# Kernel tuning notes

Hardware: AMD Instinct MI355X
Metric: run time of the kernel (lower is better)

## Reference

```python
import jax, jax.numpy as jnp
import numpy as np

N = 50000      # nodes
E = 800000     # edges (avg degree 16)
DIN = 256      # input_dim
DH = 128       # hidden_dim
ALPHA_LOGIT = 0.6190392084062235  # logit(0.65)


def setup_inputs() -> dict:
    key = jax.random.key(0)
    ks = jax.random.split(key, 12)
    f = lambda k, s: jax.random.normal(k, s, dtype=jnp.float32)
    return {
        "x": f(ks[0], (N, DIN)),
        "edge_index": jax.random.randint(ks[1], (2, E), 0, N, dtype=jnp.int32),
        "reranker_scores": f(ks[2], (N,)),
        # input_proj
        "Wp": f(ks[3], (DIN, DH)) * 0.02, "bp": jnp.zeros((DH,), jnp.float32),
        # SAGEConv 0: lin_l (aggregated neighbors, with bias), lin_r (root, no bias)
        "Wl0": f(ks[4], (DIN, DH)) * 0.02, "bl0": jnp.zeros((DH,), jnp.float32),
        "Wr0": f(ks[5], (DIN, DH)) * 0.02,
        # SAGEConv 1
        "Wl1": f(ks[6], (DH, DH)) * 0.02, "bl1": jnp.zeros((DH,), jnp.float32),
        "Wr1": f(ks[7], (DH, DH)) * 0.02,
        # score head MLP
        "W1": f(ks[8], (DH, DH // 2)) * 0.02, "b1": jnp.zeros((DH // 2,), jnp.float32),
        "W2": f(ks[9], (DH // 2, 1)) * 0.02, "b2": jnp.zeros((1,), jnp.float32),
        "alpha_logit": jnp.float32(ALPHA_LOGIT),
    }


def _sage_conv(h, src, dst, Wl, bl, Wr):
    # PyG SAGEConv (aggr='mean', root_weight=True):
    # out = lin_l(mean_{j in N(i)} h_j) + lin_r(h_i)
    msg = h[src]                                             # [E, d] gather
    agg = jax.ops.segment_sum(msg, dst, num_segments=N)      # [N, d]
    cnt = jax.ops.segment_sum(jnp.ones((src.shape[0],), h.dtype), dst, num_segments=N)
    agg = agg / jnp.maximum(cnt, 1.0)[:, None]               # mean; isolated nodes -> 0
    return agg @ Wl + bl + h @ Wr


def reference(x, edge_index, reranker_scores, Wp, bp, Wl0, bl0, Wr0,
              Wl1, bl1, Wr1, W1, b1, W2, b2, alpha_logit):
    src, dst = edge_index[0], edge_index[1]
    # norm_type='none' -> no input normalization; eval mode -> dropout is identity
    residual = x @ Wp + bp                                   # [N, DH]
    h = jax.nn.relu(_sage_conv(x, src, dst, Wl0, bl0, Wr0)) + residual
    h = jax.nn.relu(_sage_conv(h, src, dst, Wl1, bl1, Wr1)) + h
    gnn_scores = (jax.nn.relu(h @ W1 + b1) @ W2 + b2)[:, 0]  # [N]
    alpha = jax.nn.sigmoid(alpha_logit)
    return alpha * reranker_scores + (1.0 - alpha) * gnn_scores
```

## Files before the change

kernel.cpp:

```cpp
#include <hip/hip_runtime.h>
#include <hip/hip_bf16.h>


#define DIN 256
#define DH 128
#define NPB 256
#define LOG_NPB 8
#define NBMAX 256
#define EPB 2048
#define JL (EPB/256)
#define SLOTS 8192

typedef __attribute__((ext_vector_type(8))) short short8;
typedef __attribute__((ext_vector_type(4))) float float4v;
typedef __attribute__((ext_vector_type(2))) float float2v;

__device__ inline ushort f2b(float f){
  unsigned u = __float_as_uint(f);
  u = (u + 0x7fffu + ((u >> 16) & 1u)) >> 16;
  return (ushort)u;
}
__device__ inline float blo(unsigned v){ return __uint_as_float(v << 16); }
__device__ inline float bhi(unsigned v){ return __uint_as_float(v & 0xffff0000u); }
__device__ inline short8 pack8(float4 f0, float4 f1){
  short8 v;
  v[0]=(short)f2b(f0.x); v[1]=(short)f2b(f0.y); v[2]=(short)f2b(f0.z); v[3]=(short)f2b(f0.w);
  v[4]=(short)f2b(f1.x); v[5]=(short)f2b(f1.y); v[6]=(short)f2b(f1.z); v[7]=(short)f2b(f1.w);
  return v;
}
__device__ inline void glds16(const ushort* g, ushort* l){
  __builtin_amdgcn_global_load_lds((const __attribute__((address_space(1))) void*)g,
                                   (__attribute__((address_space(3))) void*)l, 16, 0, 0);
}
__device__ inline unsigned char enc8(float v){
  return (unsigned char)(__builtin_amdgcn_cvt_pk_fp8_f32(v, v, 0, false) & 0xFF);
}
__device__ inline float2v dec8(unsigned u){
  return __builtin_amdgcn_cvt_pk_f32_fp8((int)u, false);
}

__device__ inline void gather16x2(const ushort* __restrict__ a8,
    const int* __restrict__ adj, int pA, int eA, int pB, int eB, int lane,
    float& a0A, float& a1A, float& a0B, float& a1B)
{
  while (pA < eA || pB < eB){
    ushort uA[16], uB[16];
    bool dA = pA < eA, dB = pB < eB;
    if (dA){
      #pragma unroll
      for (int j=0;j<16;j++) uA[j] = a8[(size_t)adj[pA+j]*64 + lane];
    }
    if (dB){
      #pragma unroll
      for (int j=0;j<16;j++) uB[j] = a8[(size_t)adj[pB+j]*64 + lane];
    }
    if (dA){
      #pragma unroll
      for (int j=0;j<16;j++){ float2v f = dec8(uA[j]); a0A += f[0]; a1A += f[1]; }
      pA += 16;
    }
    if (dB){
      #pragma unroll
      for (int j=0;j<16;j++){ float2v f = dec8(uB[j]); a0B += f[0]; a1B += f[1]; }
      pB += 16;
    }
  }
}

__global__ __launch_bounds__(256) void fused_front(
    const float* __restrict__ x, int N, ushort* __restrict__ xb, int nstripe,
    const float* __restrict__ Wp, const float* __restrict__ Wl0, const float* __restrict__ Wr0,
    const float* __restrict__ Wl1, const float* __restrict__ Wr1, const float* __restrict__ W1,
    ushort* __restrict__ Wpf, ushort* __restrict__ Wl0f, ushort* __restrict__ Wr0f,
    ushort* __restrict__ Wl1f, ushort* __restrict__ Wr1f, ushort* __restrict__ W1f,
    const int* __restrict__ src, const int* __restrict__ dst, int E, int NB,
    int* __restrict__ bucketCnt, int* __restrict__ pairS, int* __restrict__ pairD,
    int nPart, int nConv)
{
  __shared__ int hist[NBMAX], lbase[NBMAX], gbase[NBMAX], lcur[NBMAX], sc[NBMAX];
  __shared__ int ls[EPB], ld[EPB];
  int bid = blockIdx.x;
  int t = threadIdx.x;

  if (bid < nPart){
    int base = bid * EPB;
    int cntE = E - base; if (cntE > EPB) cntE = EPB;
    for (int i=t;i<NB;i+=256) hist[i]=0;
    __syncthreads();
    int myS[JL], myD[JL];
    #pragma unroll
    for (int j=0;j<JL;j++){
      int e = base + j*256 + t;
      if (e < E){ myS[j]=src[e]; myD[j]=dst[e]; atomicAdd(&hist[myD[j]>>LOG_NPB],1); }
      else myD[j] = -1;
    }
    __syncthreads();
    if (t < NBMAX) sc[t] = (t < NB)? hist[t] : 0;
    __syncthreads();
    for (int st=1; st<NBMAX; st<<=1){
      int v = 0;
      if (t < NBMAX && t >= st) v = sc[t-st];
      __syncthreads();
      if (t < NBMAX) sc[t] += v;
      __syncthreads();
    }
    if (t < NB){
      int excl = (t>0)? sc[t-1] : 0;
      lbase[t] = excl; lcur[t] = excl;
      gbase[t] = atomicAdd(&bucketCnt[t], hist[t]);
    }
    __syncthreads();
    #pragma unroll
    for (int j=0;j<JL;j++){
      if (myD[j] >= 0){
        int b = myD[j] >> LOG_NPB;
        int p = atomicAdd(&lcur[b], 1);
        ls[p] = myS[j]; ld[p] = myD[j];
      }
    }
    __syncthreads();
    for (int i=t;i<cntE;i+=256){
      int d = ld[i];
      int b = d >> LOG_NPB;
      int p = gbase[b] + (i - lbase[b]);
      if (p < SLOTS){
        pairS[(size_t)b*SLOTS + p] = ls[i];
        pairD[(size_t)b*SLOTS + p] = d;
      }
    }
  } else if (bid < nPart + nConv){
    int gi = (bid - nPart)*256 + t;
    if (gi < nstripe*512){
      int L = gi & 63, ks = (gi>>6)&7, s = gi>>9;
      int row = s*16 + (L&15);
      int k = ks*32 + (L>>4)*8;
      short8 v;
      if (row < N){
        const float* p = x + (size_t)row*DIN + k;
        v = pack8(*(const float4*)p, *(const float4*)(p+4));
      } else {
        #pragma unroll
        for (int j=0;j<8;j++) v[j]=0;
      }
      *(short8*)(xb + (size_t)gi*8) = v;
    }
  } else {
    int gi = (bid - nPart - nConv)*256 + t;
    if (gi < 17408){
      const float* sw; ushort* dw; int cols, b0;
      if      (gi <  4096){ sw=Wp;  dw=Wpf;  cols=128; b0=0; }
      else if (gi <  8192){ sw=Wl0; dw=Wl0f; cols=128; b0=4096; }
      else if (gi < 12288){ sw=Wr0; dw=Wr0f; cols=128; b0=8192; }
      else if (gi < 14336){ sw=Wl1; dw=Wl1f; cols=128; b0=12288; }
      else if (gi < 16384){ sw=Wr1; dw=Wr1f; cols=128; b0=14336; }
      else                { sw=W1;  dw=W1f;  cols=64;  b0=16384; }
      int i = gi - b0;
      int ln = i & 63, g = i >> 6;
      int ntq = cols >> 4;
      int nt = g % ntq, ks = g / ntq;
      int col = nt*16 + (ln & 15);
      int k0 = ks*32 + (ln >> 4)*8;
      short8 v;
      #pragma unroll
      for (int j=0;j<8;j++) v[j] = (short)f2b(sw[(size_t)(k0+j)*cols + col]);
      *(short8*)(dw + (size_t)i*8) = v;
    }
  }
}

__global__ __launch_bounds__(256) void gemm0_csr(
    const ushort* __restrict__ xb, int N, int nstripe, int ngemm, int nbuck,
    const ushort* __restrict__ Wpf, const ushort* __restrict__ Wl0f, const ushort* __restrict__ Wr0f,
    const float* __restrict__ bp,
    ushort* __restrict__ xp, unsigned char* __restrict__ q8, ushort* __restrict__ xr0,
    const int* __restrict__ bucketCnt, const int* __restrict__ pairS, const int* __restrict__ pairD,
    int* __restrict__ off, int* __restrict__ deg, int* __restrict__ adj)
{
  __shared__ __align__(16) ushort smem[32768];
  int bid = blockIdx.x, t = threadIdx.x;

  if (bid >= nbuck){
    int g = bid - nbuck;
    int xcd = g & 7, jj = g >> 3;
    int mat = jj % 3;
    int b = xcd + 8*(jj/3);
    int nblk = ngemm / 3;
    const ushort* Wf = (mat==0)? Wpf : (mat==1)? Wl0f : Wr0f;
    int w = t>>6, lane = t&63, lq = lane&15, quad = lane>>4;
    #pragma unroll
    for (int j=0;j<16;j++){
      int gg = w + j*4;
      glds16(Wf + (size_t)gg*512 + lane*8, smem + gg*512);
    }
    __syncthreads();
    float bias[8];
    #pragma unroll
    for (int nt=0;nt<8;nt++) bias[nt] = (mat==0)? bp[nt*16 + lq] : 0.f;
    int nchunk = (nstripe + 3) >> 2;

#define LOADAV(AV, cc) do { \
    int stripe_ = (cc)*4 + w; \
    if (stripe_ < nstripe){ \
      _Pragma("unroll") \
      for (int ks=0;ks<8;ks++) \
        AV[ks] = *(const short8*)(xb + ((size_t)stripe_*8 + ks)*512 + lane*8); \
    } \
  } while(0)

#define COMPSTORE(AV, cc) do { \
    int stripe_ = (cc)*4 + w; \
    if (stripe_ < nstripe){ \
      int row0_ = stripe_*16; \
      float4v acc_[8]; \
      _Pragma("unroll") for (int nt=0;nt<8;nt++){ \
        _Pragma("unroll") for (int r=0;r<4;r++) acc_[nt][r]=0.f; } \
      _Pragma("unroll") for (int ks=0;ks<8;ks++){ \
        _Pragma("unroll") for (int nt=0;nt<8;nt++){ \
          short8 bf_ = *(const short8*)(smem + (size_t)((ks*8+nt)*64 + lane)*8); \
          acc_[nt] = __builtin_amdgcn_mfma_f32_16x16x32_bf16(AV[ks], bf_, acc_[nt], 0,0,0); \
        } \
      } \
      if (mat == 1){ \
        _Pragma("unroll") for (int nt=0;nt<8;nt++) \
        _Pragma("unroll") for (int r=0;r<4;r++){ \
          int row_ = row0_ + quad*4 + r; \
          if (row_ < N) q8[(size_t)row_*128 + nt*16 + lq] = enc8(acc_[nt][r]); \
        } \
      } else { \
        ushort* Y_ = (mat==0)? xp : xr0; \
        _Pragma("unroll") for (int nt=0;nt<8;nt++) \
        _Pragma("unroll") for (int r=0;r<4;r++){ \
          int row_ = row0_ + quad*4 + r; \
          if (row_ < N) Y_[(size_t)row_*128 + nt*16 + lq] = f2b(acc_[nt][r] + bias[nt]); \
        } \
      } \
    } \
  } while(0)

    short8 avA[8], avB[8];
    int c = b;
    if (c < nchunk){
      LOADAV(avA, c);
      while (true){
        int cn = c + nblk;
        if (cn < nchunk) LOADAV(avB, cn);
        COMPSTORE(avA, c);
        c = cn;
        if (c >= nchunk) break;
        cn = c + nblk;
        if (cn < nchunk) LOADAV(avA, cn);
        COMPSTORE(avB, c);
        c = cn;
        if (c >= nchunk) break;
      }
    }
#undef LOADAV
#undef COMPSTORE
  } else {
    int b = bid;
    int* cnt  = (int*)smem;
    int* offl = cnt + 256;
    int* s1   = offl + 257;
    int* win  = s1 + 256;
    int node0 = b * NPB;
    int base  = b * SLOTS;
    int ce = bucketCnt[b]; if (ce > SLOTS) ce = SLOTS;
    int ce4 = ce & ~3;
    cnt[t] = 0;
    __syncthreads();
    for (int i = t*4; i < ce4; i += 1024){
      int4 dd = *(const int4*)(pairD + base + i);
      atomicAdd(&cnt[dd.x - node0], 1);
      atomicAdd(&cnt[dd.y - node0], 1);
      atomicAdd(&cnt[dd.z - node0], 1);
      atomicAdd(&cnt[dd.w - node0], 1);
    }
    for (int i = ce4 + t; i < ce; i += 256)
      atomicAdd(&cnt[pairD[(size_t)base+i] - node0], 1);
    __syncthreads();
    int a = cnt[t];
    int pa = (a + 15) & ~15;
    s1[t] = pa;
    __syncthreads();
    for (int st=1; st<256; st<<=1){
      int v = (t>=st)? s1[t-st] : 0;
      __syncthreads();
      s1[t] += v;
      __syncthreads();
    }
    int excl = (t>0)? s1[t-1] : 0;
    offl[t] = excl;
    int ptotal = s1[255]; if (ptotal > SLOTS) ptotal = SLOTS;
    int node = node0 + t;
    if (node < N){ off[node] = base + excl; deg[node] = a; }
    __syncthreads();
    for (int i=t;i<ptotal;i+=256) win[i] = N;
    __syncthreads();
    for (int i = t*4; i < ce4; i += 1024){
      int4 dd = *(const int4*)(pairD + base + i);
      int4 ss = *(const int4*)(pairS + base + i);
      int p0 = atomicAdd(&offl[dd.x - node0], 1); if (p0 < SLOTS) win[p0] = ss.x;
      int p1 = atomicAdd(&offl[dd.y - node0], 1); if (p1 < SLOTS) win[p1] = ss.y;
      int p2 = atomicAdd(&offl[dd.z - node0], 1); if (p2 < SLOTS) win[p2] = ss.z;
      int p3 = atomicAdd(&offl[dd.w - node0], 1); if (p3 < SLOTS) win[p3] = ss.w;
    }
    for (int i = ce4 + t; i < ce; i += 256){
      int dd = pairD[(size_t)base+i];
      int p = atomicAdd(&offl[dd - node0], 1);
      if (p < SLOTS) win[p] = pairS[(size_t)base+i];
    }
    __syncthreads();
    for (int i=t;i<ptotal;i+=256) adj[(size_t)base+i] = win[i];
  }
}

__global__ __launch_bounds__(256) void combine0_f8(
    const unsigned char* __restrict__ agg8, const ushort* __restrict__ rootsrc,
    const ushort* __restrict__ ressrc, const float* __restrict__ bias,
    const int* __restrict__ off, const int* __restrict__ deg,
    const int* __restrict__ adj, ushort* __restrict__ out, int n)
{
  int t = threadIdx.x;
  int d = t & 63, w = t >> 6;
  int nA = blockIdx.x*8 + w*2, nB = nA + 1;
  if (nA >= n) return;
  const ushort* a8 = (const ushort*)agg8;
  bool vB = nB < n;
  unsigned rtA = ((const unsigned*)rootsrc)[(size_t)nA*64 + d];
  unsigned rsA = ((const unsigned*)ressrc)[(size_t)nA*64 + d];
  unsigned rtB = 0, rsB = 0;
  int pA = off[nA], cA = deg[nA], eA = pA + ((cA + 15) & ~15);
  int pB = 0, cB = 0, eB = 0;
  if (vB){
    rtB = ((const unsigned*)rootsrc)[(size_t)nB*64 + d];
    rsB = ((const unsigned*)ressrc)[(size_t)nB*64 + d];
    pB = off[nB]; cB = deg[nB]; eB = pB + ((cB + 15) & ~15);
  }
  float a0A=0.f, a1A=0.f, a0B=0.f, a1B=0.f;
  gather16x2(a8, adj, pA, eA, pB, eB, d, a0A, a1A, a0B, a1B);
  float b0 = bias[2*d], b1v = bias[2*d+1];
  float invA = 1.f / (float)((cA > 1)? cA : 1);
  float o0 = fmaxf(a0A*invA + b0  + blo(rtA), 0.f) + blo(rsA);
  float o1 = fmaxf(a1A*invA + b1v + bhi(rtA), 0.f) + bhi(rsA);
  ((unsigned*)out)[(size_t)nA*64 + d] = (unsigned)f2b(o0) | ((unsigned)f2b(o1) << 16);
  if (vB){
    float invB = 1.f / (float)((cB > 1)? cB : 1);
    float q0 = fmaxf(a0B*invB + b0  + blo(rtB), 0.f) + blo(rsB);
    float q1 = fmaxf(a1B*invB + b1v + bhi(rtB), 0.f) + bhi(rsB);
    ((unsigned*)out)[(size_t)nB*64 + d] = (unsigned)f2b(q0) | ((unsigned)f2b(q1) << 16);
  }
}

__global__ __launch_bounds__(256) void gemm1_wres(
    const ushort* __restrict__ h, int N,
    const ushort* __restrict__ Wl1f, const ushort* __restrict__ Wr1f,
    unsigned char* __restrict__ q8, ushort* __restrict__ hr1)
{
  __shared__ __align__(16) ushort Bs[32768];
  int t = threadIdx.x, w = t>>6, lane = t&63, lq = lane&15, quad = lane>>4;
  int tile = blockIdx.x;
  #pragma unroll
  for (int j=0;j<16;j++){
    int r = w + j*4;
    int m = r>>5, g = r&31;
    const ushort* Wm = m ? Wr1f : Wl1f;
    glds16(Wm + (size_t)g*512 + lane*8, Bs + r*512);
  }
  short8 av[2][4];
  int row0 = tile*128 + w*32;
  #pragma unroll
  for (int mt=0;mt<2;mt++){
    int row = row0 + mt*16 + lq; if (row >= N) row = N-1;
    #pragma unroll
    for (int ks=0;ks<4;ks++)
      av[mt][ks] = *(const short8*)(h + (size_t)row*128 + ks*32 + quad*8);
  }
  __syncthreads();
  #pragma unroll
  for (int m=0;m<2;m++){
    float4v acc[2][8];
    #pragma unroll
    for (int i=0;i<2;i++)
      #pragma unroll
      for (int j=0;j<8;j++)
        #pragma unroll
        for (int r=0;r<4;r++) acc[i][j][r] = 0.f;
    #pragma unroll
    for (int ks=0;ks<4;ks++){
      #pragma unroll
      for (int nt=0;nt<8;nt++){
        short8 bf = *(const short8*)(Bs + ((m*32 + ks*8 + nt)*64 + lane)*8);
        acc[0][nt] = __builtin_amdgcn_mfma_f32_16x16x32_bf16(av[0][ks], bf, acc[0][nt], 0,0,0);
        acc[1][nt] = __builtin_amdgcn_mfma_f32_16x16x32_bf16(av[1][ks], bf, acc[1][nt], 0,0,0);
      }
    }
    #pragma unroll
    for (int mt=0;mt<2;mt++){
      #pragma unroll
      for (int r=0;r<4;r++){
        int row = row0 + mt*16 + quad*4 + r;
        if (row < N){
          if (m == 0){
            #pragma unroll
            for (int nt=0;nt<8;nt++)
              q8[(size_t)row*128 + nt*16 + lq] = enc8(acc[mt][nt][r]);
          } else {
            #pragma unroll
            for (int nt=0;nt<8;nt++)
              hr1[(size_t)row*128 + nt*16 + lq] = f2b(acc[mt][nt][r]);
          }
        }
      }
    }
  }
}

__global__ __launch_bounds__(256) void combine1_head(
    const unsigned char* __restrict__ agg8, const ushort* __restrict__ hr1,
    const ushort* __restrict__ h, const float* __restrict__ bl1,
    const int* __restrict__ off, const int* __restrict__ deg, const int* __restrict__ adj,
    const ushort* __restrict__ W1f, const float* __restrict__ b1,
    const float* __restrict__ W2, const float* __restrict__ b2,
    const float* __restrict__ alogit, const float* __restrict__ rer,
    float* __restrict__ out, int n)
{
  __shared__ __align__(16) ushort W1s[8192];
  __shared__ __align__(16) ushort h2s[16*136];
  int t = threadIdx.x, w = t>>6, lane = t&63, lq = lane&15, quad = lane>>4;
  #pragma unroll
  for (int j=0;j<4;j++){
    int g = w + j*4;
    glds16(W1f + (size_t)g*512 + lane*8, W1s + g*512);
  }
  int node0 = blockIdx.x*16;
  unsigned* h2u = (unsigned*)h2s;
  const ushort* a8 = (const ushort*)agg8;
  float bb0 = bl1[2*lane], bb1 = bl1[2*lane+1];
  #pragma unroll
  for (int jp=0;jp<2;jp++){
    int nA = node0 + w*4 + jp*2, nB = nA + 1;
    bool vA = nA < n, vB = nB < n;
    unsigned rtA=0, rsA=0, rtB=0, rsB=0;
    int pA=0, eA=0, cA=0, pB=0, eB=0, cB=0;
    if (vA){
      rtA = ((const unsigned*)hr1)[(size_t)nA*64 + lane];
      rsA = ((const unsigned*)h  )[(size_t)nA*64 + lane];
      pA = off[nA]; cA = deg[nA]; eA = pA + ((cA + 15) & ~15);
    }
    if (vB){
      rtB = ((const unsigned*)hr1)[(size_t)nB*64 + lane];
      rsB = ((const unsigned*)h  )[(size_t)nB*64 + lane];
      pB = off[nB]; cB = deg[nB]; eB = pB + ((cB + 15) & ~15);
    }
    float a0A=0.f, a1A=0.f, a0B=0.f, a1B=0.f;
    gather16x2(a8, adj, pA, eA, pB, eB, lane, a0A, a1A, a0B, a1B);
    float o0A=0.f, o1A=0.f, o0B=0.f, o1B=0.f;
    if (vA){
      float inv = 1.f / (float)((cA > 1)? cA : 1);
      o0A = fmaxf(a0A*inv + bb0 + blo(rtA), 0.f) + blo(rsA);
      o1A = fmaxf(a1A*inv + bb1 + bhi(rtA), 0.f) + bhi(rsA);
    }
    if (vB){
      float inv = 1.f / (float)((cB > 1)? cB : 1);
      o0B = fmaxf(a0B*inv + bb0 + blo(rtB), 0.f) + blo(rsB);
      o1B = fmaxf(a1B*inv + bb1 + bhi(rtB), 0.f) + bhi(rsB);
    }
    h2u[(w*4 + jp*2    )*68 + lane] = (unsigned)f2b(o0A) | ((unsigned)f2b(o1A) << 16);
    h2u[(w*4 + jp*2 + 1)*68 + lane] = (unsigned)f2b(o0B) | ((unsigned)f2b(o1B) << 16);
  }
  __syncthreads();

  short8 av[4];
  #pragma unroll
  for (int ks=0;ks<4;ks++)
    av[ks] = *(const short8*)(h2s + lq*136 + ks*32 + quad*8);
  float4v acc[4];
  #pragma unroll
  for (int nt=0;nt<4;nt++)
    #pragma unroll
    for (int r=0;r<4;r++) acc[nt][r] = 0.f;
  #pragma unroll
  for (int ks=0;ks<4;ks++){
    #pragma unroll
    for (int nt=0;nt<4;nt++){
      short8 bf = *(const short8*)(W1s + ((ks*4 + nt)*64 + lane)*8);
      acc[nt] = __builtin_amdgcn_mfma_f32_16x16x32_bf16(av[ks], bf, acc[nt], 0,0,0);
    }
  }
  float al = alogit[0];
  float a  = 1.f / (1.f + __expf(-al));
  float pw[4] = {0.f,0.f,0.f,0.f};
  #pragma unroll
  for (int nt=0; nt<4; nt++){
    int c = nt*16 + lq;
    float w2 = W2[c];
    float bb = b1[c];
    #pragma unroll
    for (int r=0; r<4; r++)
      pw[r] += fmaxf(acc[nt][r] + bb, 0.f) * w2;
  }
  #pragma unroll
  for (int mask=1; mask<16; mask<<=1){
    #pragma unroll
    for (int r=0; r<4; r++)
      pw[r] += __shfl_xor(pw[r], mask);
  }
  if (lq == 0){
    #pragma unroll
    for (int r=0; r<4; r++){
      int rl = quad*4 + r;
      if ((rl >> 2) == w){
        int node = node0 + rl;
        if (node < n)
          out[node] = a * rer[node] + (1.f - a) * (pw[r] + b2[0]);
      }
    }
  }
}

extern "C" void kernel_launch(void* const* d_in, const int* in_sizes, int n_in,
                              void* d_out, int out_size, void* d_ws, size_t ws_size,
                              hipStream_t stream)
{
  (void)n_in; (void)out_size; (void)ws_size;
  const float* x    = (const float*)d_in[0];
  const int*   ei   = (const int*)d_in[1];
  const float* rer  = (const float*)d_in[2];
  const float* Wp   = (const float*)d_in[3];
  const float* bp   = (const float*)d_in[4];
  const float* Wl0  = (const float*)d_in[5];
  const float* bl0  = (const float*)d_in[6];
  const float* Wr0  = (const float*)d_in[7];
  const float* Wl1  = (const float*)d_in[8];
  const float* bl1  = (const float*)d_in[9];
  const float* Wr1  = (const float*)d_in[10];
  const float* W1   = (const float*)d_in[11];
  const float* b1   = (const float*)d_in[12];
  const float* W2   = (const float*)d_in[13];
  const float* b2   = (const float*)d_in[14];
  const float* alogit = (const float*)d_in[15];

  const int N = in_sizes[2];
  const int E = in_sizes[1] / 2;
  const int* src = ei;
  const int* dst = ei + E;
  const int NB = (N + NPB - 1) / NPB;
  const int nstripe = (N + 15) / 16;
  const int ntile = (N + 127) / 128;
  const int nPart = (E + EPB - 1) / EPB;
  const int nConv = (nstripe*512 + 255)/256;

  ushort* U = (ushort*)d_ws;
  ushort* xb  = U;
  ushort* xp  = xb + (size_t)nstripe*512*8;
  ushort* xr0 = xp  + (size_t)N*DH;
  ushort* h   = xr0 + (size_t)N*DH;
  unsigned char* q8 = (unsigned char*)(h + (size_t)N*DH);
  ushort* Wpf  = (ushort*)(q8 + (size_t)(N+1)*DH);
  ushort* Wl0f = Wpf  + (size_t)4096*8;
  ushort* Wr0f = Wl0f + (size_t)4096*8;
  ushort* Wl1f = Wr0f + (size_t)4096*8;
  ushort* Wr1f = Wl1f + (size_t)2048*8;
  ushort* W1f  = Wr1f + (size_t)2048*8;
  int* I = (int*)(W1f + (size_t)1024*8);
  int* bucketCnt = I;
  int* off   = bucketCnt + NBMAX;
  int* deg   = off + N;
  int* pairS = deg + N;
  int* pairD = pairS + (size_t)NB*SLOTS;
  int* adj   = pairD + (size_t)NB*SLOTS;

  hipMemsetAsync(bucketCnt, 0, NBMAX*sizeof(int), stream);
  hipMemsetAsync(q8 + (size_t)N*DH, 0, DH, stream);

  fused_front<<<nPart + nConv + 68, 256, 0, stream>>>(
      x, N, xb, nstripe, Wp, Wl0, Wr0, Wl1, Wr1, W1,
      Wpf, Wl0f, Wr0f, Wl1f, Wr1f, W1f,
      src, dst, E, NB, bucketCnt, pairS, pairD, nPart, nConv);

  gemm0_csr<<<NB + 768, 256, 0, stream>>>(
      xb, N, nstripe, 768, NB, Wpf, Wl0f, Wr0f, bp, xp, q8, xr0,
      bucketCnt, pairS, pairD, off, deg, adj);

  combine0_f8<<<(N+7)/8, 256, 0, stream>>>(q8, xr0, xp, bl0, off, deg, adj, h, N);

  gemm1_wres<<<ntile, 256, 0, stream>>>(h, N, Wl1f, Wr1f, q8, xr0);

  combine1_head<<<(N+15)/16, 256, 0, stream>>>(
      q8, xr0, h, bl1, off, deg, adj, W1f, b1, W2, b2, alogit, rer, (float*)d_out, N);
}
```

Baseline: 228.0 us.

## Split each wavefront into half-waves gathering 4-byte fp8 rows per lane

```diff
diff --git a/kernel.cpp b/kernel.cpp
--- a/kernel.cpp
+++ b/kernel.cpp
@@ -35,35 +35,47 @@
 __device__ inline unsigned char enc8(float v){
   return (unsigned char)(__builtin_amdgcn_cvt_pk_fp8_f32(v, v, 0, false) & 0xFF);
 }
-__device__ inline float2v dec8(unsigned u){
+__device__ inline float2v dec8lo(unsigned u){
   return __builtin_amdgcn_cvt_pk_f32_fp8((int)u, false);
 }
-
-__device__ inline void gather16x2(const ushort* __restrict__ a8,
-    const int* __restrict__ adj, int pA, int eA, int pB, int eB, int lane,
-    float& a0A, float& a1A, float& a0B, float& a1B)
+__device__ inline float2v dec8hi(unsigned u){
+  return __builtin_amdgcn_cvt_pk_f32_fp8((int)u, true);
+}
+
+__device__ inline void gather_sw(const unsigned* __restrict__ a8u,
+    const int* __restrict__ adj, int zrow, int ln,
+    int pP, int eP, int pQ, int eQ,
+    float* accP, float* accQ)
 {
-  while (pA < eA || pB < eB){
-    ushort uA[16], uB[16];
-    bool dA = pA < eA, dB = pB < eB;
-    if (dA){
-      #pragma unroll
-      for (int j=0;j<16;j++) uA[j] = a8[(size_t)adj[pA+j]*64 + lane];
-    }
-    if (dB){
-      #pragma unroll
-      for (int j=0;j<16;j++) uB[j] = a8[(size_t)adj[pB+j]*64 + lane];
-    }
-    if (dA){
-      #pragma unroll
-      for (int j=0;j<16;j++){ float2v f = dec8(uA[j]); a0A += f[0]; a1A += f[1]; }
-      pA += 16;
-    }
-    if (dB){
-      #pragma unroll
-      for (int j=0;j<16;j++){ float2v f = dec8(uB[j]); a0B += f[0]; a1B += f[1]; }
-      pB += 16;
-    }
+  int rem = eP - pP; int remQ = eQ - pQ; if (remQ > rem) rem = remQ;
+  #pragma unroll
+  for (int m=1; m<64; m<<=1){ int o = __shfl_xor(rem, m); if (o > rem) rem = o; }
+  int iters = rem >> 4;
+  for (int it=0; it<iters; ++it){
+    bool aP = pP < eP, aQ = pQ < eQ;
+    unsigned uP[16], uQ[16];
+    #pragma unroll
+    for (int j=0;j<16;j++){
+      int ix = zrow; if (aP) ix = adj[pP+j];
+      uP[j] = a8u[(size_t)ix*32 + ln];
+    }
+    #pragma unroll
+    for (int j=0;j<16;j++){
+      int ix = zrow; if (aQ) ix = adj[pQ+j];
+      uQ[j] = a8u[(size_t)ix*32 + ln];
+    }
+    #pragma unroll
+    for (int j=0;j<16;j++){
+      float2v f0 = dec8lo(uP[j]), f1 = dec8hi(uP[j]);
+      accP[0]+=f0[0]; accP[1]+=f0[1]; accP[2]+=f1[0]; accP[3]+=f1[1];
+    }
+    #pragma unroll
+    for (int j=0;j<16;j++){
+      float2v f0 = dec8lo(uQ[j]), f1 = dec8hi(uQ[j]);
+      accQ[0]+=f0[0]; accQ[1]+=f0[1]; accQ[2]+=f1[0]; accQ[3]+=f1[1];
+    }
+    if (aP) pP += 16;
+    if (aQ) pQ += 16;
   }
 }
 
@@ -320,34 +332,49 @@
     const int* __restrict__ off, const int* __restrict__ deg,
     const int* __restrict__ adj, ushort* __restrict__ out, int n)
 {
-  int t = threadIdx.x;
-  int d = t & 63, w = t >> 6;
-  int nA = blockIdx.x*8 + w*2, nB = nA + 1;
-  if (nA >= n) return;
-  const ushort* a8 = (const ushort*)agg8;
-  bool vB = nB < n;
-  unsigned rtA = ((const unsigned*)rootsrc)[(size_t)nA*64 + d];
-  unsigned rsA = ((const unsigned*)ressrc)[(size_t)nA*64 + d];
-  unsigned rtB = 0, rsB = 0;
-  int pA = off[nA], cA = deg[nA], eA = pA + ((cA + 15) & ~15);
-  int pB = 0, cB = 0, eB = 0;
-  if (vB){
-    rtB = ((const unsigned*)rootsrc)[(size_t)nB*64 + d];
-    rsB = ((const unsigned*)ressrc)[(size_t)nB*64 + d];
-    pB = off[nB]; cB = deg[nB]; eB = pB + ((cB + 15) & ~15);
-  }
-  float a0A=0.f, a1A=0.f, a0B=0.f, a1B=0.f;
-  gather16x2(a8, adj, pA, eA, pB, eB, d, a0A, a1A, a0B, a1B);
-  float b0 = bias[2*d], b1v = bias[2*d+1];
-  float invA = 1.f / (float)((cA > 1)? cA : 1);
-  float o0 = fmaxf(a0A*invA + b0  + blo(rtA), 0.f) + blo(rsA);
-  float o1 = fmaxf(a1A*invA + b1v + bhi(rtA), 0.f) + bhi(rsA);
-  ((unsigned*)out)[(size_t)nA*64 + d] = (unsigned)f2b(o0) | ((unsigned)f2b(o1) << 16);
-  if (vB){
-    float invB = 1.f / (float)((cB > 1)? cB : 1);
-    float q0 = fmaxf(a0B*invB + b0  + blo(rtB), 0.f) + blo(rsB);
-    float q1 = fmaxf(a1B*invB + b1v + bhi(rtB), 0.f) + bhi(rsB);
-    ((unsigned*)out)[(size_t)nB*64 + d] = (unsigned)f2b(q0) | ((unsigned)f2b(q1) << 16);
+  int t = threadIdx.x, w = t>>6, lane = t&63, ln = lane&31, sel = lane>>5;
+  int nbase = blockIdx.x*16 + w*4;
+  if (nbase >= n) return;
+  int n0 = nbase + sel;
+  int n1 = nbase + 2 + sel;
+  const unsigned* a8u = (const unsigned*)agg8;
+  bool v0 = n0 < n, v1 = n1 < n;
+  int p0=0,c0=0,e0=0,p1=0,c1=0,e1=0;
+  uint2 rt0={0,0}, rs0={0,0}, rt1={0,0}, rs1={0,0};
+  if (v0){
+    p0 = off[n0]; c0 = deg[n0]; e0 = p0 + ((c0+15)&~15);
+    rt0 = ((const uint2*)rootsrc)[(size_t)n0*32 + ln];
+    rs0 = ((const uint2*)ressrc)[(size_t)n0*32 + ln];
+  }
+  if (v1){
+    p1 = off[n1]; c1 = deg[n1]; e1 = p1 + ((c1+15)&~15);
+    rt1 = ((const uint2*)rootsrc)[(size_t)n1*32 + ln];
+    rs1 = ((const uint2*)ressrc)[(size_t)n1*32 + ln];
+  }
+  float accP[4]={0.f,0.f,0.f,0.f}, accQ[4]={0.f,0.f,0.f,0.f};
+  gather_sw(a8u, adj, n, ln, p0, e0, p1, e1, accP, accQ);
+  float4 bv = *(const float4*)(bias + 4*ln);
+  if (v0){
+    float inv = 1.f / (float)((c0 > 1)? c0 : 1);
+    float o0 = fmaxf(accP[0]*inv + bv.x + blo(rt0.x), 0.f) + blo(rs0.x);
+    float o1 = fmaxf(accP[1]*inv + bv.y + bhi(rt0.x), 0.f) + bhi(rs0.x);
+    float o2 = fmaxf(accP[2]*inv + bv.z + blo(rt0.y), 0.f) + blo(rs0.y);
+    float o3 = fmaxf(accP[3]*inv + bv.w + bhi(rt0.y), 0.f) + bhi(rs0.y);
+    uint2 ov;
+    ov.x = (unsigned)f2b(o0) | ((unsigned)f2b(o1) << 16);
+    ov.y = (unsigned)f2b(o2) | ((unsigned)f2b(o3) << 16);
+    ((uint2*)out)[(size_t)n0*32 + ln] = ov;
+  }
+  if (v1){
+    float inv = 1.f / (float)((c1 > 1)? c1 : 1);
+    float o0 = fmaxf(accQ[0]*inv + bv.x + blo(rt1.x), 0.f) + blo(rs1.x);
+    float o1 = fmaxf(accQ[1]*inv + bv.y + bhi(rt1.x), 0.f) + bhi(rs1.x);
+    float o2 = fmaxf(accQ[2]*inv + bv.z + blo(rt1.y), 0.f) + blo(rs1.y);
+    float o3 = fmaxf(accQ[3]*inv + bv.w + bhi(rt1.y), 0.f) + bhi(rs1.y);
+    uint2 ov;
+    ov.x = (unsigned)f2b(o0) | ((unsigned)f2b(o1) << 16);
+    ov.y = (unsigned)f2b(o2) | ((unsigned)f2b(o3) << 16);
+    ((uint2*)out)[(size_t)n1*32 + ln] = ov;
   }
 }
 
@@ -427,6 +454,7 @@
   __shared__ __align__(16) ushort W1s[8192];
   __shared__ __align__(16) ushort h2s[16*136];
   int t = threadIdx.x, w = t>>6, lane = t&63, lq = lane&15, quad = lane>>4;
+  int ln = lane&31, sel = lane>>5;
   #pragma unroll
   for (int j=0;j<4;j++){
     int g = w + j*4;
@@ -434,39 +462,52 @@
   }
   int node0 = blockIdx.x*16;
   unsigned* h2u = (unsigned*)h2s;
-  const ushort* a8 = (const ushort*)agg8;
-  float bb0 = bl1[2*lane], bb1 = bl1[2*lane+1];
-  #pragma unroll
-  for (int jp=0;jp<2;jp++){
-    int nA = node0 + w*4 + jp*2, nB = nA + 1;
-    bool vA = nA < n, vB = nB < n;
-    unsigned rtA=0, rsA=0, rtB=0, rsB=0;
-    int pA=0, eA=0, cA=0, pB=0, eB=0, cB=0;
-    if (vA){
-      rtA = ((const unsigned*)hr1)[(size_t)nA*64 + lane];
-      rsA = ((const unsigned*)h  )[(size_t)nA*64 + lane];
-      pA = off[nA]; cA = deg[nA]; eA = pA + ((cA + 15) & ~15);
-    }
-    if (vB){
-      rtB = ((const unsigned*)hr1)[(size_t)nB*64 + lane];
-      rsB = ((const unsigned*)h  )[(size_t)nB*64 + lane];
-      pB = off[nB]; cB = deg[nB]; eB = pB + ((cB + 15) & ~15);
-    }
-    float a0A=0.f, a1A=0.f, a0B=0.f, a1B=0.f;
-    gather16x2(a8, adj, pA, eA, pB, eB, lane, a0A, a1A, a0B, a1B);
-    float o0A=0.f, o1A=0.f, o0B=0.f, o1B=0.f;
-    if (vA){
-      float inv = 1.f / (float)((cA > 1)? cA : 1);
-      o0A = fmaxf(a0A*inv + bb0 + blo(rtA), 0.f) + blo(rsA);
-      o1A = fmaxf(a1A*inv + bb1 + bhi(rtA), 0.f) + bhi(rsA);
-    }
-    if (vB){
-      float inv = 1.f / (float)((cB > 1)? cB : 1);
-      o0B = fmaxf(a0B*inv + bb0 + blo(rtB), 0.f) + blo(rsB);
-      o1B = fmaxf(a1B*inv + bb1 + bhi(rtB), 0.f) + bhi(rsB);
-    }
-    h2u[(w*4 + jp*2    )*68 + lane] = (unsigned)f2b(o0A) | ((unsigned)f2b(o1A) << 16);
-    h2u[(w*4 + jp*2 + 1)*68 + lane] = (unsigned)f2b(o0B) | ((unsigned)f2b(o1B) << 16);
+  const unsigned* a8u = (const unsigned*)agg8;
+
+  int nbase = node0 + w*4;
+  int n0 = nbase + sel;
+  int n1 = nbase + 2 + sel;
+  bool v0 = n0 < n, v1 = n1 < n;
+  int p0=0,c0=0,e0=0,p1=0,c1=0,e1=0;
+  uint2 rt0={0,0}, rs0={0,0}, rt1={0,0}, rs1={0,0};
+  if (v0){
+    p0 = off[n0]; c0 = deg[n0]; e0 = p0 + ((c0+15)&~15);
+    rt0 = ((const uint2*)hr1)[(size_t)n0*32 + ln];
+    rs0 = ((const uint2*)h  )[(size_t)n0*32 + ln];
+  }
+  if (v1){
+    p1 = off[n1]; c1 = deg[n1]; e1 = p1 + ((c1+15)&~15);
+    rt1 = ((const uint2*)hr1)[(size_t)n1*32 + ln];
+    rs1 = ((const uint2*)h  )[(size_t)n1*32 + ln];
+  }
+  float accP[4]={0.f,0.f,0.f,0.f}, accQ[4]={0.f,0.f,0.f,0.f};
+  gather_sw(a8u, adj, n, ln, p0, e0, p1, e1, accP, accQ);
+  float4 bv = *(const float4*)(bl1 + 4*ln);
+  {
+    float o0=0.f,o1=0.f,o2=0.f,o3=0.f;
+    if (v0){
+      float inv = 1.f / (float)((c0 > 1)? c0 : 1);
+      o0 = fmaxf(accP[0]*inv + bv.x + blo(rt0.x), 0.f) + blo(rs0.x);
+      o1 = fmaxf(accP[1]*inv + bv.y + bhi(rt0.x), 0.f) + bhi(rs0.x);
+      o2 = fmaxf(accP[2]*inv + bv.z + blo(rt0.y), 0.f) + blo(rs0.y);
+      o3 = fmaxf(accP[3]*inv + bv.w + bhi(rt0.y), 0.f) + bhi(rs0.y);
+    }
+    int r = w*4 + sel;
+    h2u[r*68 + 2*ln  ] = (unsigned)f2b(o0) | ((unsigned)f2b(o1) << 16);
+    h2u[r*68 + 2*ln+1] = (unsigned)f2b(o2) | ((unsigned)f2b(o3) << 16);
+  }
+  {
+    float o0=0.f,o1=0.f,o2=0.f,o3=0.f;
+    if (v1){
+      float inv = 1.f / (float)((c1 > 1)? c1 : 1);
+      o0 = fmaxf(accQ[0]*inv + bv.x + blo(rt1.x), 0.f) + blo(rs1.x);
+      o1 = fmaxf(accQ[1]*inv + bv.y + bhi(rt1.x), 0.f) + bhi(rs1.x);
+      o2 = fmaxf(accQ[2]*inv + bv.z + blo(rt1.y), 0.f) + blo(rs1.y);
+      o3 = fmaxf(accQ[3]*inv + bv.w + bhi(rt1.y), 0.f) + bhi(rs1.y);
+    }
+    int r = w*4 + 2 + sel;
+    h2u[r*68 + 2*ln  ] = (unsigned)f2b(o0) | ((unsigned)f2b(o1) << 16);
+    h2u[r*68 + 2*ln+1] = (unsigned)f2b(o2) | ((unsigned)f2b(o3) << 16);
   }
   __syncthreads();
 
@@ -582,7 +623,7 @@
       xb, N, nstripe, 768, NB, Wpf, Wl0f, Wr0f, bp, xp, q8, xr0,
       bucketCnt, pairS, pairD, off, deg, adj);
 
-  combine0_f8<<<(N+7)/8, 256, 0, stream>>>(q8, xr0, xp, bl0, off, deg, adj, h, N);
+  combine0_f8<<<(N+15)/16, 256, 0, stream>>>(q8, xr0, xp, bl0, off, deg, adj, h, N);
 
   gemm1_wres<<<ntile, 256, 0, stream>>>(h, N, Wl1f, Wr1f, q8, xr0);
 
```

Result: slower. 309.0 us (+35.5%).
